# Kernel optimization log

Measured on AMD Instinct MI355X. Metric: run time of the kernel, lower is better.

## Reference

```python
import jax, jax.numpy as jnp
import numpy as np

B, G, N, P, E, F, K = 8, 256, 1024, 4, 1, 256, 4
ZERO_TOL = 1e-9
INF = 1e12
ATT_SLOPE = 0.2  # leaky relu slope inside attention


def setup_inputs() -> dict:
    key = jax.random.key(0)
    ks = jax.random.split(key, 6)
    stdv = float(1.0 / np.sqrt(G * P))
    x = jax.random.normal(ks[0], (B, G, N), jnp.float32)
    mixer = jax.random.uniform(ks[1], (P, E, 2 * F), jnp.float32, -stdv, stdv)
    weight = jax.random.uniform(ks[2], (P, E, F, G), jnp.float32, -stdv, stdv)
    weight_bias = jnp.zeros((P, E, F), jnp.float32)  # reset_parameters inits to 0
    filterWeight = jax.random.uniform(ks[3], (P, F, E, K, G), jnp.float32, -stdv, stdv)
    bias = jax.random.uniform(ks[4], (F, 1), jnp.float32, -stdv, stdv)
    adj = (jax.random.uniform(ks[5], (B, E, N, N)) < 0.05).astype(jnp.float32)
    S = jnp.maximum(adj, jnp.eye(N, dtype=jnp.float32)[None, None])
    return dict(x=x, mixer=mixer, weight=weight, weight_bias=weight_bias,
                filterWeight=filterWeight, bias=bias, S=S)


def reference(x, mixer, weight, weight_bias, filterWeight, bias, S):
    # --- learnAttentionGSOBatch ---
    # Wx: [B,P,E,F,N]
    Wx = jnp.einsum('pefg,bgn->bpefn', weight, x) + weight_bias[None, :, :, :, None]
    a1 = mixer[..., :F]   # [P,E,F]
    a2 = mixer[..., F:]   # [P,E,F]
    e1 = jnp.einsum('pef,bpefn->bpen', a1, Wx)  # a1^T W x_j
    e2 = jnp.einsum('pef,bpefn->bpen', a2, Wx)  # a2^T W x_i
    # aWx[b,p,e,i,j] = e1[j] + e2[i]  (matches a1Wx + a2Wx^T broadcast)
    aWx = e1[..., None, :] + e2[..., :, None]   # [B,P,E,N,N]
    eij = jax.nn.leaky_relu(aWx, ATT_SLOPE)
    mask = (jnp.sum(jnp.abs(S), axis=1)[:, None, None] > ZERO_TOL).astype(x.dtype)  # [B,1,1,N,N]
    aij = jax.nn.softmax(eij * mask - (1.0 - mask) * INF, axis=-1) * mask  # [B,P,E,N,N]

    # --- K-hop polynomial filter ---
    xk = jnp.broadcast_to(x[:, None, None], (B, P, E, G, N))
    zs = [xk]
    for _ in range(1, K):
        xk = jnp.matmul(xk, aij)        # diffuse along attention GSO
        zs.append(xk)
    z = jnp.stack(zs, axis=3)            # [B,P,E,K,G,N]
    # h reshape [P,F,E*K*G] contracted against z reshaped [B,P,N,E*K*G]
    y = jnp.einsum('bpekgn,pfekg->bpfn', z, filterWeight) + bias  # bias [F,1] broadcasts

    # --- forward wrapper: nonlinearity (leaky_relu, default slope 0.01) + head concat ---
    y = jax.nn.leaky_relu(y)                              # [B,P,F,N]
    y = jnp.transpose(y, (0, 3, 1, 2)).reshape(B, N, P * F)
    return jnp.transpose(y, (0, 2, 1))                    # [B, P*F, N]
```

## Files before the change

kernel.cpp:

```cpp
#include <hip/hip_runtime.h>
#include <hip/hip_bf16.h>

#define B_ 8
#define G_ 256
#define N_ 1024
#define P_ 4
#define F_ 256
#define KHOP 4
#define KG_ (KHOP * G_)


typedef unsigned short ushort_t;
typedef __bf16 bf16x8 __attribute__((ext_vector_type(8)));
typedef unsigned short u16x8 __attribute__((ext_vector_type(8)));
typedef float f32x4 __attribute__((ext_vector_type(4)));

__device__ __forceinline__ unsigned short f2bf(float f) {
  union { float fl; unsigned int i; } v; v.fl = f;
  return (unsigned short)((v.i + 0x7fffu + ((v.i >> 16) & 1u)) >> 16);
}

__device__ __forceinline__ void gload_lds16(const ushort_t* g, ushort_t* l) {
  __builtin_amdgcn_global_load_lds(
      (const __attribute__((address_space(1))) void*)g,
      (__attribute__((address_space(3))) void*)l, 16, 0, 0);
}

__global__ __launch_bounds__(256) void k_prep(
    const float* __restrict__ x, const float* __restrict__ mixer,
    const float* __restrict__ weight, const float* __restrict__ wb,
    const float* __restrict__ fw, float* __restrict__ e1, float* __restrict__ e2,
    ushort_t* __restrict__ fwbf, ushort_t* __restrict__ xT,
    float* __restrict__ sumb) {
  int blk = blockIdx.x;
  int t = threadIdx.x;
  if (blk < 128) {
    __shared__ float s1[G_], s2[G_];
    __shared__ float cred[2][4];
    int bp = blk >> 2;
    int nc = blk & 3;
    int b = bp >> 2, p = bp & (P_ - 1);
    int n = nc * 256 + t;
    float acc1 = 0.f, acc2 = 0.f;
    const float* wp = weight + (size_t)p * F_ * G_ + t;
    const float* mp = mixer + p * 2 * F_;
    for (int f = 0; f < F_; ++f) {
      float wv = wp[(size_t)f * G_];
      acc1 = fmaf(mp[f], wv, acc1);
      acc2 = fmaf(mp[F_ + f], wv, acc2);
    }
    s1[t] = acc1;
    s2[t] = acc2;
    float c1p = mp[t] * wb[p * F_ + t];
    float c2p = mp[F_ + t] * wb[p * F_ + t];
#pragma unroll
    for (int mask = 1; mask < 64; mask <<= 1) {
      c1p += __shfl_xor(c1p, mask, 64);
      c2p += __shfl_xor(c2p, mask, 64);
    }
    if ((t & 63) == 0) {
      cred[0][t >> 6] = c1p;
      cred[1][t >> 6] = c2p;
    }
    __syncthreads();
    float c1 = cred[0][0] + cred[0][1] + cred[0][2] + cred[0][3];
    float c2 = cred[1][0] + cred[1][1] + cred[1][2] + cred[1][3];
    const float* xb = x + (size_t)b * G_ * N_ + n;
    float a1 = 0.f, a2 = 0.f;
#pragma unroll 8
    for (int g = 0; g < G_; ++g) {
      float xv = xb[(size_t)g * N_];
      a1 = fmaf(s1[g], xv, a1);
      a2 = fmaf(s2[g], xv, a2);
    }
    e1[(size_t)bp * N_ + n] = c1 + a1;
    e2[(size_t)bp * N_ + n] = c2 + a2;
  } else if (blk < 256) {
    int tile = blk - 128;
    int p = tile >> 5;
    int mb = (tile >> 4) & 1;
    int kb = tile & 15;
    int w = t >> 6, lane = t & 63;
    size_t tbase = ((size_t)(p * 2 + mb) * 16 + kb) * 8192;
#pragma unroll
    for (int q = 0; q < 4; ++q) {
      int cell = q * 4 + w;
      int f = mb * 128 + (cell >> 1) * 16 + (lane & 15);
      int kg = kb * 64 + (cell & 1) * 32 + (lane >> 4) * 8;
      const float* s = fw + ((size_t)p * F_ + f) * KG_ + kg;
      float4 v0 = *(const float4*)&s[0];
      float4 v1 = *(const float4*)&s[4];
      u16x8 o;
      o[0] = f2bf(v0.x); o[1] = f2bf(v0.y); o[2] = f2bf(v0.z); o[3] = f2bf(v0.w);
      o[4] = f2bf(v1.x); o[5] = f2bf(v1.y); o[6] = f2bf(v1.z); o[7] = f2bf(v1.w);
      *(u16x8*)&fwbf[tbase + (size_t)cell * 512 + lane * 8] = o;
    }
  } else if (blk < 768) {
    __shared__ ushort_t tile[64][66];
    int idx = blk - 256;
    int n0 = (idx & 15) * 64;
    int g0 = ((idx >> 4) & 3) * 64;
    int b = idx >> 6;
    int rr = t >> 4, cc = (t & 15) * 4;
#pragma unroll
    for (int ps = 0; ps < 4; ++ps) {
      float4 v = *(const float4*)&x[((size_t)b * G_ + g0 + ps * 16 + rr) * N_ + n0 + cc];
      tile[ps * 16 + rr][cc] = f2bf(v.x);
      tile[ps * 16 + rr][cc + 1] = f2bf(v.y);
      tile[ps * 16 + rr][cc + 2] = f2bf(v.z);
      tile[ps * 16 + rr][cc + 3] = f2bf(v.w);
    }
    __syncthreads();
    int w = t >> 6, lane = t & 63;
    int nb = n0 >> 7;
    int kb = g0 >> 6;
    int rhalf = (n0 & 64) >> 4;
    size_t tbase = ((size_t)(b * 8 + nb) * 4 + kb) * 8192;
#pragma unroll
    for (int q = 0; q < 2; ++q) {
      int cl = q * 4 + w;
      int cell = (rhalf + (cl >> 1)) * 2 + (cl & 1);
      int nl = (cl >> 1) * 16 + (lane & 15);
      int gl = (cl & 1) * 32 + (lane >> 4) * 8;
      u16x8 v;
#pragma unroll
      for (int j = 0; j < 8; ++j) v[j] = tile[gl + j][nl];
      *(u16x8*)&xT[tbase + (size_t)cell * 512 + lane * 8] = v;
    }
  } else {
    int i = (blk - 768) * 256 + t;
    sumb[i] = 0.f;
  }
}

__global__ __launch_bounds__(256) void k_att(const float* __restrict__ e1,
                                             const float* __restrict__ e2,
                                             const float* __restrict__ S,
                                             ushort_t* __restrict__ expT,
                                             float* __restrict__ sumb) {
  __shared__ ushort_t tile[256][72];
  __shared__ float se1[P_][256];
  __shared__ float se2[P_][64];
  int b = blockIdx.z;
  int i0 = blockIdx.y * 64;
  int j0 = blockIdx.x * 256;
  int t = threadIdx.x;
  int rr = t >> 4;
  int cc4 = t & 15;
  int cc = cc4 * 4;

#pragma unroll
  for (int p = 0; p < P_; ++p) {
    int bp = b * 4 + p;
    se1[p][t] = e1[(size_t)bp * N_ + j0 + t];
    if (t < 64) se2[p][t] = e2[(size_t)bp * N_ + i0 + t];
  }
  __syncthreads();

  const float* Sb = S + (size_t)b * N_ * N_;
  unsigned long long mbits = 0ull;
#pragma unroll
  for (int js = 0; js < 4; ++js) {
#pragma unroll
    for (int ps = 0; ps < 4; ++ps) {
      int il = ps * 16 + rr;
      float4 s4 = *(const float4*)&Sb[(size_t)(i0 + il) * N_ + j0 + js * 64 + cc];
      float sv[4] = {s4.x, s4.y, s4.z, s4.w};
#pragma unroll
      for (int s = 0; s < 4; ++s)
        if (fabsf(sv[s]) > 1e-9f)
          mbits |= 1ull << (js * 16 + ps * 4 + s);
    }
  }

  int w = t >> 6, lane = t & 63;
  int kb = i0 >> 6;
  for (int p = 0; p < P_; ++p) {
    int bp = b * 4 + p;
    float re2[4];
#pragma unroll
    for (int ps = 0; ps < 4; ++ps) re2[ps] = se2[p][ps * 16 + rr];
    float psum[4] = {0.f, 0.f, 0.f, 0.f};
#pragma unroll
    for (int js = 0; js < 4; ++js) {
      float4 e1q = *(float4*)&se1[p][js * 64 + cc];
      float e1v[4] = {e1q.x, e1q.y, e1q.z, e1q.w};
#pragma unroll
      for (int ps = 0; ps < 4; ++ps) {
        int il = ps * 16 + rr;
#pragma unroll
        for (int s = 0; s < 4; ++s) {
          float v = e1v[s] + re2[ps];
          float l = v >= 0.f ? v : 0.2f * v;
          bool m = (mbits >> (js * 16 + ps * 4 + s)) & 1ull;
          float e = m ? __expf(l) : 0.f;
          psum[ps] += e;
          tile[js * 64 + cc + s][il] = f2bf(e);
        }
      }
    }
#pragma unroll
    for (int mask = 1; mask < 16; mask <<= 1) {
#pragma unroll
      for (int ps = 0; ps < 4; ++ps) psum[ps] += __shfl_xor(psum[ps], mask, 64);
    }
    if (cc4 == 0) {
#pragma unroll
      for (int ps = 0; ps < 4; ++ps)
        atomicAdd(&sumb[(size_t)bp * N_ + i0 + ps * 16 + rr], psum[ps]);
    }
    __syncthreads();
#pragma unroll
    for (int hb = 0; hb < 2; ++hb) {
      size_t tbase = ((size_t)(bp * 8 + (j0 >> 7) + hb) * 16 + kb) * 8192;
#pragma unroll
      for (int q = 0; q < 4; ++q) {
        int cell = q * 4 + w;
        int r = (cell >> 1) * 16 + (lane & 15);
        int il = (cell & 1) * 32 + (lane >> 4) * 8;
        u16x8 v = *(const u16x8*)&tile[hb * 128 + r][il];
        *(u16x8*)&expT[tbase + (size_t)cell * 512 + lane * 8] = v;
      }
    }
    __syncthreads();
  }
}

__global__ __launch_bounds__(256, 3) void gemm_step(
    const ushort_t* __restrict__ Aprev, const ushort_t* __restrict__ Bt,
    const ushort_t* __restrict__ fwbf, const ushort_t* __restrict__ xT,
    const float* __restrict__ bias, const float* __restrict__ sumb,
    ushort_t* __restrict__ outb, float* __restrict__ outf,
    int kslice, int has_prev, int last) {
  __shared__ ushort_t Bs[2][8192];
  int id = blockIdx.x;
  int xcd = id & 7;
  int slot = id >> 3;
  int bp = xcd * 4 + (slot >> 4);
  int inner = slot & 15;
  int mb = inner >> 3;
  int m0 = mb * 128;
  int nb = inner & 7;
  int n0 = nb * 128;
  int p = bp & (P_ - 1), b = bp >> 2;
  int t = threadIdx.x;
  int lane = t & 63;
  int w = t >> 6;
  int wm = w >> 1, wn = w & 1;
  int lr = lane & 15, quad = lane >> 4;

  const ushort_t* A1 = has_prev ? (Aprev + (size_t)(bp * 2 + mb) * 16 * 8192) : fwbf;
  const ushort_t* A2 = fwbf + ((size_t)(p * 2 + mb) * 16 + kslice * 4) * 8192;
  const ushort_t* B1 = Bt + (size_t)(bp * 8 + nb) * 16 * 8192;
  const ushort_t* B2 = xT + (size_t)(b * 8 + nb) * 4 * 8192;

  const int ntA = has_prev ? (N_ / 64) : 0;
  const int NT = ntA + G_ / 64;

  f32x4 acc[4][4] = {};
  int laneoff = lane * 8;

  auto stageB = [&](int it, int buf) {
    const ushort_t* Bb = (it < ntA) ? B1 + (size_t)it * 8192
                                    : B2 + (size_t)(it - ntA) * 8192;
#pragma unroll
    for (int l = 0; l < 4; ++l) {
      int coff = (w * 4 + l) * 512;
      gload_lds16(Bb + coff + laneoff, &Bs[buf][coff]);
    }
  };

  stageB(0, 0);
  int cur = 0;
  for (int it = 0; it < NT; ++it) {
    const ushort_t* At = (it < ntA) ? A1 + (size_t)it * 8192
                                    : A2 + (size_t)(it - ntA) * 8192;
    u16x8 afr[2][4];
#pragma unroll
    for (int c = 0; c < 2; ++c)
#pragma unroll
      for (int mi = 0; mi < 4; ++mi)
        afr[c][mi] = *(const u16x8*)&At[(((wm * 4 + mi) * 2) + c) * 512 + laneoff];
    __builtin_amdgcn_sched_barrier(0);
    if (it + 1 < NT) {
      stageB(it + 1, cur ^ 1);
      asm volatile("s_waitcnt vmcnt(12)" ::: "memory");
    } else {
      asm volatile("s_waitcnt vmcnt(0)" ::: "memory");
    }
    __builtin_amdgcn_s_barrier();
#pragma unroll
    for (int c = 0; c < 2; ++c) {
      bf16x8 bfr[4];
#pragma unroll
      for (int ni = 0; ni < 4; ++ni)
        bfr[ni] = __builtin_bit_cast(bf16x8,
            *(const u16x8*)&Bs[cur][(((wn * 4 + ni) * 2) + c) * 512 + lane * 8]);
#pragma unroll
      for (int mi = 0; mi < 4; ++mi) {
        bf16x8 af = __builtin_bit_cast(bf16x8, afr[c][mi]);
#pragma unroll
        for (int ni = 0; ni < 4; ++ni)
          acc[mi][ni] = __builtin_amdgcn_mfma_f32_16x16x32_bf16(af, bfr[ni], acc[mi][ni], 0, 0, 0);
      }
    }
    __builtin_amdgcn_s_barrier();
    cur ^= 1;
  }

  if (last) {
    float* Ob = outf + (size_t)bp * (F_ * N_);
#pragma unroll
    for (int mi = 0; mi < 4; ++mi) {
      int fbase = m0 + wm * 64 + mi * 16 + quad * 4;
#pragma unroll
      for (int ni = 0; ni < 4; ++ni) {
        int n = n0 + wn * 64 + ni * 16 + lr;
#pragma unroll
        for (int r = 0; r < 4; ++r) {
          float v = acc[mi][ni][r] + bias[fbase + r];
          Ob[(size_t)(fbase + r) * N_ + n] = v >= 0.f ? v : 0.01f * v;
        }
      }
    }
  } else {
    ushort_t* scratch = &Bs[0][0];
    float iv[4];
#pragma unroll
    for (int ni = 0; ni < 4; ++ni)
      iv[ni] = 1.0f / sumb[(size_t)bp * N_ + n0 + wn * 64 + ni * 16 + lr];
#pragma unroll
    for (int mi = 0; mi < 4; ++mi) {
#pragma unroll
      for (int ni = 0; ni < 4; ++ni) {
        int nL = wn * 64 + ni * 16 + lr;
        int kbh = nL >> 6;
        int kloc = nL & 63;
        int cellbase = kbh * 8192 +
                       ((wm * 4 + mi) * 2 + (kloc >> 5)) * 512 +
                       (((kloc >> 3) & 3) * 16 + quad * 4) * 8 + (kloc & 7);
#pragma unroll
        for (int r = 0; r < 4; ++r)
          scratch[cellbase + r * 8] = f2bf(acc[mi][ni][r] * iv[ni]);
      }
    }
    __syncthreads();
    size_t obase = ((size_t)(bp * 2 + mb) * 16 + (n0 >> 6)) * 8192;
#pragma unroll
    for (int pass = 0; pass < 8; ++pass) {
      int fl = pass * 2048 + t * 8;
      *(u16x8*)&outb[obase + fl] = *(const u16x8*)&scratch[fl];
    }
  }
}

extern "C" void kernel_launch(void* const* d_in, const int* in_sizes, int n_in,
                              void* d_out, int out_size, void* d_ws, size_t ws_size,
                              hipStream_t stream) {
  const float* x = (const float*)d_in[0];
  const float* mixer = (const float*)d_in[1];
  const float* weight = (const float*)d_in[2];
  const float* wb = (const float*)d_in[3];
  const float* fw = (const float*)d_in[4];
  const float* bias = (const float*)d_in[5];
  const float* S = (const float*)d_in[6];
  float* out = (float*)d_out;

  char* ws = (char*)d_ws;
  size_t off = 0;
  auto take = [&](size_t bytes) -> char* {
    char* p = ws + off;
    off = (off + bytes + 255) & ~(size_t)255;
    return p;
  };
  float* e1 = (float*)take((size_t)B_ * P_ * N_ * 4);
  float* e2 = (float*)take((size_t)B_ * P_ * N_ * 4);
  float* sumb = (float*)take((size_t)B_ * P_ * N_ * 4);
  ushort_t* fwbf = (ushort_t*)take((size_t)P_ * F_ * KHOP * G_ * 2);
  ushort_t* xT = (ushort_t*)take((size_t)B_ * N_ * G_ * 2);
  ushort_t* expT = (ushort_t*)take((size_t)B_ * P_ * N_ * N_ * 2);
  ushort_t* sA = (ushort_t*)take((size_t)B_ * P_ * F_ * N_ * 2);
  ushort_t* sB = (ushort_t*)take((size_t)B_ * P_ * F_ * N_ * 2);

  k_prep<<<896, 256, 0, stream>>>(x, mixer, weight, wb, fw, e1, e2, fwbf, xT, sumb);
  k_att<<<dim3(4, 16, 8), 256, 0, stream>>>(e1, e2, S, expT, sumb);

  gemm_step<<<512, 256, 0, stream>>>(nullptr, expT, fwbf, xT, bias, sumb, sA, nullptr, 3, 0, 0);
  gemm_step<<<512, 256, 0, stream>>>(sA, expT, fwbf, xT, bias, sumb, sB, nullptr, 2, 1, 0);
  gemm_step<<<512, 256, 0, stream>>>(sB, expT, fwbf, xT, bias, sumb, sA, nullptr, 1, 1, 0);
  gemm_step<<<512, 256, 0, stream>>>(sA, expT, fwbf, xT, bias, sumb, nullptr, out, 0, 1, 1);
}
```

Measured before the change: 225.4 us.

## Load B fragments directly from global into registers, dropping LDS staging

The gemm_step kernel no longer stages B tiles into double-buffered LDS with global_load_lds and block barriers. Each wave now loads both A and B fragments straight from global memory into registers, the loop is unrolled by two, and the launch-bounds occupancy hint drops from 3 to 2. This removes the barrier synchronisation and LDS round-trip, but B tiles are now fetched once per wave instead of once per block, which doubles B global and L2 traffic. Latency hiding depends on loop unrolling rather than explicit prefetch.

Result: slower. 255.7 us (+13.4%).

```diff
diff --git a/kernel.cpp b/kernel.cpp
--- a/kernel.cpp
+++ b/kernel.cpp
@@ -18,12 +18,6 @@
 __device__ __forceinline__ unsigned short f2bf(float f) {
   union { float fl; unsigned int i; } v; v.fl = f;
   return (unsigned short)((v.i + 0x7fffu + ((v.i >> 16) & 1u)) >> 16);
-}
-
-__device__ __forceinline__ void gload_lds16(const ushort_t* g, ushort_t* l) {
-  __builtin_amdgcn_global_load_lds(
-      (const __attribute__((address_space(1))) void*)g,
-      (__attribute__((address_space(3))) void*)l, 16, 0, 0);
 }
 
 __global__ __launch_bounds__(256) void k_prep(
@@ -226,13 +220,13 @@
   }
 }
 
-__global__ __launch_bounds__(256, 3) void gemm_step(
+__global__ __launch_bounds__(256, 2) void gemm_step(
     const ushort_t* __restrict__ Aprev, const ushort_t* __restrict__ Bt,
     const ushort_t* __restrict__ fwbf, const ushort_t* __restrict__ xT,
     const float* __restrict__ bias, const float* __restrict__ sumb,
     ushort_t* __restrict__ outb, float* __restrict__ outf,
     int kslice, int has_prev, int last) {
-  __shared__ ushort_t Bs[2][8192];
+  __shared__ ushort_t scratch[16384];
   int id = blockIdx.x;
   int xcd = id & 7;
   int slot = id >> 3;
@@ -259,53 +253,39 @@
 
   f32x4 acc[4][4] = {};
   int laneoff = lane * 8;
-
-  auto stageB = [&](int it, int buf) {
-    const ushort_t* Bb = (it < ntA) ? B1 + (size_t)it * 8192
-                                    : B2 + (size_t)(it - ntA) * 8192;
-#pragma unroll
-    for (int l = 0; l < 4; ++l) {
-      int coff = (w * 4 + l) * 512;
-      gload_lds16(Bb + coff + laneoff, &Bs[buf][coff]);
-    }
-  };
-
-  stageB(0, 0);
-  int cur = 0;
+  int aoff[2][4], boff[2][4];
+#pragma unroll
+  for (int c = 0; c < 2; ++c)
+#pragma unroll
+    for (int i = 0; i < 4; ++i) {
+      aoff[c][i] = (((wm * 4 + i) * 2) + c) * 512 + laneoff;
+      boff[c][i] = (((wn * 4 + i) * 2) + c) * 512 + laneoff;
+    }
+
+#pragma unroll 2
   for (int it = 0; it < NT; ++it) {
     const ushort_t* At = (it < ntA) ? A1 + (size_t)it * 8192
                                     : A2 + (size_t)(it - ntA) * 8192;
-    u16x8 afr[2][4];
+    const ushort_t* Bp = (it < ntA) ? B1 + (size_t)it * 8192
+                                    : B2 + (size_t)(it - ntA) * 8192;
+    u16x8 afr[2][4], bfr[2][4];
 #pragma unroll
     for (int c = 0; c < 2; ++c)
 #pragma unroll
-      for (int mi = 0; mi < 4; ++mi)
-        afr[c][mi] = *(const u16x8*)&At[(((wm * 4 + mi) * 2) + c) * 512 + laneoff];
-    __builtin_amdgcn_sched_barrier(0);
-    if (it + 1 < NT) {
-      stageB(it + 1, cur ^ 1);
-      asm volatile("s_waitcnt vmcnt(12)" ::: "memory");
-    } else {
-      asm volatile("s_waitcnt vmcnt(0)" ::: "memory");
-    }
-    __builtin_amdgcn_s_barrier();
-#pragma unroll
-    for (int c = 0; c < 2; ++c) {
-      bf16x8 bfr[4];
-#pragma unroll
-      for (int ni = 0; ni < 4; ++ni)
-        bfr[ni] = __builtin_bit_cast(bf16x8,
-            *(const u16x8*)&Bs[cur][(((wn * 4 + ni) * 2) + c) * 512 + lane * 8]);
+      for (int i = 0; i < 4; ++i) {
+        afr[c][i] = *(const u16x8*)&At[aoff[c][i]];
+        bfr[c][i] = *(const u16x8*)&Bp[boff[c][i]];
+      }
+#pragma unroll
+    for (int c = 0; c < 2; ++c)
 #pragma unroll
       for (int mi = 0; mi < 4; ++mi) {
         bf16x8 af = __builtin_bit_cast(bf16x8, afr[c][mi]);
 #pragma unroll
         for (int ni = 0; ni < 4; ++ni)
-          acc[mi][ni] = __builtin_amdgcn_mfma_f32_16x16x32_bf16(af, bfr[ni], acc[mi][ni], 0, 0, 0);
-      }
-    }
-    __builtin_amdgcn_s_barrier();
-    cur ^= 1;
+          acc[mi][ni] = __builtin_amdgcn_mfma_f32_16x16x32_bf16(
+              af, __builtin_bit_cast(bf16x8, bfr[c][ni]), acc[mi][ni], 0, 0, 0);
+      }
   }
 
   if (last) {
@@ -324,7 +304,6 @@
       }
     }
   } else {
-    ushort_t* scratch = &Bs[0][0];
     float iv[4];
 #pragma unroll
     for (int ni = 0; ni < 4; ++ni)
```

## Fuse four Horner GEMM steps into one persistent kernel with grid barriers

Applied to the files above, without the earlier changes.

Replaces the four separate gemm_step launches with one kernel that loops over the four Horner steps. Blocks synchronise between steps through an atomic-counter grid barrier, and the counters are zeroed in k_prep. The aim is to remove three kernel launch gaps and the tail drain between dependent GEMMs. In exchange, occupancy is lowered to two blocks per CU so all 512 blocks can be co-resident. The barrier relies on that co-residency and has a guarded spin that could silently give wrong results if it times out.

Measured after the change: 647.6 us. 2.87x slower.

```diff
diff --git a/kernel.cpp b/kernel.cpp
--- a/kernel.cpp
+++ b/kernel.cpp
@@ -31,7 +31,7 @@
     const float* __restrict__ weight, const float* __restrict__ wb,
     const float* __restrict__ fw, float* __restrict__ e1, float* __restrict__ e2,
     ushort_t* __restrict__ fwbf, ushort_t* __restrict__ xT,
-    float* __restrict__ sumb) {
+    float* __restrict__ sumb, unsigned int* __restrict__ ctr) {
   int blk = blockIdx.x;
   int t = threadIdx.x;
   if (blk < 128) {
@@ -130,6 +130,7 @@
   } else {
     int i = (blk - 768) * 256 + t;
     sumb[i] = 0.f;
+    if (blk == 768 && t < 8) ctr[t] = 0u;
   }
 }
 
@@ -226,13 +227,31 @@
   }
 }
 
-__global__ __launch_bounds__(256, 3) void gemm_step(
-    const ushort_t* __restrict__ Aprev, const ushort_t* __restrict__ Bt,
-    const ushort_t* __restrict__ fwbf, const ushort_t* __restrict__ xT,
-    const float* __restrict__ bias, const float* __restrict__ sumb,
-    ushort_t* __restrict__ outb, float* __restrict__ outf,
-    int kslice, int has_prev, int last) {
+__device__ __forceinline__ void grid_barrier(unsigned int* ctr, int step,
+                                             unsigned int nblocks, int t) {
+  __threadfence();
+  __syncthreads();
+  if (t == 0) {
+    __hip_atomic_fetch_add(&ctr[step], 1u, __ATOMIC_RELEASE,
+                           __HIP_MEMORY_SCOPE_AGENT);
+    unsigned int guard = 0;
+    while (__hip_atomic_load(&ctr[step], __ATOMIC_ACQUIRE,
+                             __HIP_MEMORY_SCOPE_AGENT) < nblocks &&
+           guard < (1u << 30))
+      ++guard;
+  }
+  __syncthreads();
+  __threadfence();
+}
+
+__global__ __launch_bounds__(256, 2) void gemm_fused(
+    const ushort_t* __restrict__ Bt, const ushort_t* __restrict__ fwbf,
+    const ushort_t* __restrict__ xT, const float* __restrict__ bias,
+    const float* __restrict__ sumb, ushort_t* __restrict__ sA,
+    ushort_t* __restrict__ sB, float* __restrict__ outf,
+    unsigned int* __restrict__ ctr) {
   __shared__ ushort_t Bs[2][8192];
+
   int id = blockIdx.x;
   int xcd = id & 7;
   int slot = id >> 3;
@@ -248,108 +267,119 @@
   int w = t >> 6;
   int wm = w >> 1, wn = w & 1;
   int lr = lane & 15, quad = lane >> 4;
-
-  const ushort_t* A1 = has_prev ? (Aprev + (size_t)(bp * 2 + mb) * 16 * 8192) : fwbf;
-  const ushort_t* A2 = fwbf + ((size_t)(p * 2 + mb) * 16 + kslice * 4) * 8192;
+  int laneoff = lane * 8;
+
   const ushort_t* B1 = Bt + (size_t)(bp * 8 + nb) * 16 * 8192;
   const ushort_t* B2 = xT + (size_t)(b * 8 + nb) * 4 * 8192;
 
-  const int ntA = has_prev ? (N_ / 64) : 0;
-  const int NT = ntA + G_ / 64;
-
-  f32x4 acc[4][4] = {};
-  int laneoff = lane * 8;
-
-  auto stageB = [&](int it, int buf) {
-    const ushort_t* Bb = (it < ntA) ? B1 + (size_t)it * 8192
-                                    : B2 + (size_t)(it - ntA) * 8192;
-#pragma unroll
-    for (int l = 0; l < 4; ++l) {
-      int coff = (w * 4 + l) * 512;
-      gload_lds16(Bb + coff + laneoff, &Bs[buf][coff]);
-    }
-  };
-
-  stageB(0, 0);
-  int cur = 0;
-  for (int it = 0; it < NT; ++it) {
-    const ushort_t* At = (it < ntA) ? A1 + (size_t)it * 8192
-                                    : A2 + (size_t)(it - ntA) * 8192;
-    u16x8 afr[2][4];
-#pragma unroll
-    for (int c = 0; c < 2; ++c)
-#pragma unroll
-      for (int mi = 0; mi < 4; ++mi)
-        afr[c][mi] = *(const u16x8*)&At[(((wm * 4 + mi) * 2) + c) * 512 + laneoff];
-    __builtin_amdgcn_sched_barrier(0);
-    if (it + 1 < NT) {
-      stageB(it + 1, cur ^ 1);
-      asm volatile("s_waitcnt vmcnt(12)" ::: "memory");
+  float iv[4];
+#pragma unroll
+  for (int ni = 0; ni < 4; ++ni)
+    iv[ni] = 1.0f / sumb[(size_t)bp * N_ + n0 + wn * 64 + ni * 16 + lr];
+
+  for (int step = 0; step < 4; ++step) {
+    int kslice = 3 - step;
+    int has_prev = (step > 0);
+    int last = (step == 3);
+    const ushort_t* Aprev = (step == 2) ? sB : sA;
+    ushort_t* outb = (step == 1) ? sB : sA;
+
+    const ushort_t* A1 = has_prev ? (Aprev + (size_t)(bp * 2 + mb) * 16 * 8192) : fwbf;
+    const ushort_t* A2 = fwbf + ((size_t)(p * 2 + mb) * 16 + kslice * 4) * 8192;
+
+    const int ntA = has_prev ? (N_ / 64) : 0;
+    const int NT = ntA + G_ / 64;
+
+    f32x4 acc[4][4] = {};
+
+    auto stageB = [&](int it, int buf) {
+      const ushort_t* Bb = (it < ntA) ? B1 + (size_t)it * 8192
+                                      : B2 + (size_t)(it - ntA) * 8192;
+#pragma unroll
+      for (int l = 0; l < 4; ++l) {
+        int coff = (w * 4 + l) * 512;
+        gload_lds16(Bb + coff + laneoff, &Bs[buf][coff]);
+      }
+    };
+
+    stageB(0, 0);
+    int cur = 0;
+    for (int it = 0; it < NT; ++it) {
+      const ushort_t* At = (it < ntA) ? A1 + (size_t)it * 8192
+                                      : A2 + (size_t)(it - ntA) * 8192;
+      u16x8 afr[2][4];
+#pragma unroll
+      for (int c = 0; c < 2; ++c)
+#pragma unroll
+        for (int mi = 0; mi < 4; ++mi)
+          afr[c][mi] = *(const u16x8*)&At[(((wm * 4 + mi) * 2) + c) * 512 + laneoff];
+      __builtin_amdgcn_sched_barrier(0);
+      if (it + 1 < NT) {
+        stageB(it + 1, cur ^ 1);
+        asm volatile("s_waitcnt vmcnt(12)" ::: "memory");
+      } else {
+        asm volatile("s_waitcnt vmcnt(0)" ::: "memory");
+      }
+      __builtin_amdgcn_s_barrier();
+#pragma unroll
+      for (int c = 0; c < 2; ++c) {
+        bf16x8 bfr[4];
+#pragma unroll
+        for (int ni = 0; ni < 4; ++ni)
+          bfr[ni] = __builtin_bit_cast(bf16x8,
+              *(const u16x8*)&Bs[cur][(((wn * 4 + ni) * 2) + c) * 512 + lane * 8]);
+#pragma unroll
+        for (int mi = 0; mi < 4; ++mi) {
+          bf16x8 af = __builtin_bit_cast(bf16x8, afr[c][mi]);
+#pragma unroll
+          for (int ni = 0; ni < 4; ++ni)
+            acc[mi][ni] = __builtin_amdgcn_mfma_f32_16x16x32_bf16(af, bfr[ni], acc[mi][ni], 0, 0, 0);
+        }
+      }
+      __builtin_amdgcn_s_barrier();
+      cur ^= 1;
+    }
+
+    if (last) {
+      float* Ob = outf + (size_t)bp * (F_ * N_);
+#pragma unroll
+      for (int mi = 0; mi < 4; ++mi) {
+        int fbase = m0 + wm * 64 + mi * 16 + quad * 4;
+#pragma unroll
+        for (int ni = 0; ni < 4; ++ni) {
+          int n = n0 + wn * 64 + ni * 16 + lr;
+#pragma unroll
+          for (int r = 0; r < 4; ++r) {
+            float v = acc[mi][ni][r] + bias[fbase + r];
+            Ob[(size_t)(fbase + r) * N_ + n] = v >= 0.f ? v : 0.01f * v;
+          }
+        }
+      }
     } else {
-      asm volatile("s_waitcnt vmcnt(0)" ::: "memory");
-    }
-    __builtin_amdgcn_s_barrier();
-#pragma unroll
-    for (int c = 0; c < 2; ++c) {
-      bf16x8 bfr[4];
-#pragma unroll
-      for (int ni = 0; ni < 4; ++ni)
-        bfr[ni] = __builtin_bit_cast(bf16x8,
-            *(const u16x8*)&Bs[cur][(((wn * 4 + ni) * 2) + c) * 512 + lane * 8]);
+      ushort_t* scratch = &Bs[0][0];
 #pragma unroll
       for (int mi = 0; mi < 4; ++mi) {
-        bf16x8 af = __builtin_bit_cast(bf16x8, afr[c][mi]);
-#pragma unroll
-        for (int ni = 0; ni < 4; ++ni)
-          acc[mi][ni] = __builtin_amdgcn_mfma_f32_16x16x32_bf16(af, bfr[ni], acc[mi][ni], 0, 0, 0);
-      }
-    }
-    __builtin_amdgcn_s_barrier();
-    cur ^= 1;
-  }
-
-  if (last) {
-    float* Ob = outf + (size_t)bp * (F_ * N_);
-#pragma unroll
-    for (int mi = 0; mi < 4; ++mi) {
-      int fbase = m0 + wm * 64 + mi * 16 + quad * 4;
-#pragma unroll
-      for (int ni = 0; ni < 4; ++ni) {
-        int n = n0 + wn * 64 + ni * 16 + lr;
-#pragma unroll
-        for (int r = 0; r < 4; ++r) {
-          float v = acc[mi][ni][r] + bias[fbase + r];
-          Ob[(size_t)(fbase + r) * N_ + n] = v >= 0.f ? v : 0.01f * v;
+#pragma unroll
+        for (int ni = 0; ni < 4; ++ni) {
+          int nL = wn * 64 + ni * 16 + lr;
+          int kbh = nL >> 6;
+          int kloc = nL & 63;
+          int cellbase = kbh * 8192 +
+                         ((wm * 4 + mi) * 2 + (kloc >> 5)) * 512 +
+                         (((kloc >> 3) & 3) * 16 + quad * 4) * 8 + (kloc & 7);
+#pragma unroll
+          for (int r = 0; r < 4; ++r)
+            scratch[cellbase + r * 8] = f2bf(acc[mi][ni][r] * iv[ni]);
         }
       }
-    }
-  } else {
-    ushort_t* scratch = &Bs[0][0];
-    float iv[4];
-#pragma unroll
-    for (int ni = 0; ni < 4; ++ni)
-      iv[ni] = 1.0f / sumb[(size_t)bp * N_ + n0 + wn * 64 + ni * 16 + lr];
-#pragma unroll
-    for (int mi = 0; mi < 4; ++mi) {
-#pragma unroll
-      for (int ni = 0; ni < 4; ++ni) {
-        int nL = wn * 64 + ni * 16 + lr;
-        int kbh = nL >> 6;
-        int kloc = nL & 63;
-        int cellbase = kbh * 8192 +
-                       ((wm * 4 + mi) * 2 + (kloc >> 5)) * 512 +
-                       (((kloc >> 3) & 3) * 16 + quad * 4) * 8 + (kloc & 7);
-#pragma unroll
-        for (int r = 0; r < 4; ++r)
-          scratch[cellbase + r * 8] = f2bf(acc[mi][ni][r] * iv[ni]);
-      }
-    }
-    __syncthreads();
-    size_t obase = ((size_t)(bp * 2 + mb) * 16 + (n0 >> 6)) * 8192;
-#pragma unroll
-    for (int pass = 0; pass < 8; ++pass) {
-      int fl = pass * 2048 + t * 8;
-      *(u16x8*)&outb[obase + fl] = *(const u16x8*)&scratch[fl];
+      __syncthreads();
+      size_t obase = ((size_t)(bp * 2 + mb) * 16 + (n0 >> 6)) * 8192;
+#pragma unroll
+      for (int pass = 0; pass < 8; ++pass) {
+        int fl = pass * 2048 + t * 8;
+        *(u16x8*)&outb[obase + fl] = *(const u16x8*)&scratch[fl];
+      }
+      grid_barrier(ctr, step, 512u, t);
     }
   }
 }
@@ -381,12 +411,12 @@
   ushort_t* expT = (ushort_t*)take((size_t)B_ * P_ * N_ * N_ * 2);
   ushort_t* sA = (ushort_t*)take((size_t)B_ * P_ * F_ * N_ * 2);
   ushort_t* sB = (ushort_t*)take((size_t)B_ * P_ * F_ * N_ * 2);
-
-  k_prep<<<896, 256, 0, stream>>>(x, mixer, weight, wb, fw, e1, e2, fwbf, xT, sumb);
+  unsigned int* ctr = (unsigned int*)take(8 * sizeof(unsigned int));
+
+  k_prep<<<896, 256, 0, stream>>>(x, mixer, weight, wb, fw, e1, e2, fwbf, xT,
+                                  sumb, ctr);
   k_att<<<dim3(4, 16, 8), 256, 0, stream>>>(e1, e2, S, expT, sumb);
 
-  gemm_step<<<512, 256, 0, stream>>>(nullptr, expT, fwbf, xT, bias, sumb, sA, nullptr, 3, 0, 0);
-  gemm_step<<<512, 256, 0, stream>>>(sA, expT, fwbf, xT, bias, sumb, sB, nullptr, 2, 1, 0);
-  gemm_step<<<512, 256, 0, stream>>>(sB, expT, fwbf, xT, bias, sumb, sA, nullptr, 1, 1, 0);
-  gemm_step<<<512, 256, 0, stream>>>(sA, expT, fwbf, xT, bias, sumb, nullptr, out, 0, 1, 1);
-}
+  gemm_fused<<<512, 256, 0, stream>>>(expT, fwbf, xT, bias, sumb, sA, sB, out,
+                                      ctr);
+}
```
